# Kernel optimization log

Hardware: AMD Instinct MI355X
Metric: run time of the kernel (lower is better)

The kernel has to match this reference:

```python
import jax, jax.numpy as jnp
import numpy as np

SCOPE = 27
RICKER_WIDTH = 6.0
DAMPING = 0.12
IN_CHANNELS = 256


def _ricker(scope, std, damping):
    # mexican-hat / ricker wavelet, length `scope`, centered
    x = jnp.arange(scope, dtype=jnp.float32) - (scope // 2)
    a = 2.0 / (jnp.sqrt(3.0 * std) * jnp.pi ** 0.25)
    return damping * a * (1.0 - (x / std) ** 2) * jnp.exp(-(x ** 2) / (2.0 * std ** 2))


def _pad_roll(k, in_channels):
    # zero-pad kernel (length scope) to in_channels, roll so center sits at i=0-ish
    scope = k.shape[-1]
    pad_left = (in_channels - scope) // 2
    pad_right = in_channels - scope - pad_left
    padded = jnp.concatenate([jnp.zeros((pad_left,), k.dtype), k, jnp.zeros((pad_right,), k.dtype)])
    return jnp.roll(padded, in_channels // 2 + 1)


def _circulant(kernel, c):
    # tpl[i, j] = kernel[(j - i) mod C]  (each row is the kernel rolled by i)
    idx = (jnp.arange(c)[None, :] - jnp.arange(c)[:, None]) % c
    return kernel[idx]


def setup_inputs() -> dict:
    key = jax.random.key(0)
    k1, _ = jax.random.split(key)
    activations = jax.random.normal(k1, (32, IN_CHANNELS, 64, 64), dtype=jnp.float32)
    inhibition_filter = _ricker(SCOPE, RICKER_WIDTH, DAMPING)  # learned param, ricker init
    return {"activations": activations, "inhibition_filter": inhibition_filter}


def reference(activations, inhibition_filter):
    n, c, h, w = activations.shape
    kernel = _pad_roll(inhibition_filter, c)              # [C]
    tpl = _circulant(kernel, c)                           # [C, C]
    tpl_inv = jnp.linalg.inv(jnp.eye(c, dtype=tpl.dtype) - tpl)  # [C, C]
    # torch: (N, H*W, C) @ tpl_inv -> out[n, c_out, h, w] = sum_k act[n, k, h, w] * tpl_inv[k, c_out]
    return jnp.einsum('nkhw,kc->nchw', activations, tpl_inv)
```

## Files before the change

### kernel.cpp

```cpp
#include <hip/hip_runtime.h>
#include <hip/hip_bf16.h>

#define C 256
#define HW 4096
#define REP_ROW 528
#define LDSK 264

typedef __attribute__((ext_vector_type(8))) short short8;
typedef __attribute__((ext_vector_type(4))) float float4v;

__device__ __forceinline__ unsigned short f2bf(float x) {
    unsigned u = __builtin_bit_cast(unsigned, x);
    u = (u + 0x7fffu + ((u >> 16) & 1u)) >> 16;
    return (unsigned short)u;
}

__global__ void build_rep_kernel(const float* __restrict__ filt, unsigned short* __restrict__ rep) {
    __shared__ double twc[256], tws[256];
    __shared__ double Gre[256], Gim[256];
    __shared__ float gsh[256];
    const int t = threadIdx.x;
    const double PI = 3.14159265358979323846;
    double th = (double)t * (PI / 128.0);
    twc[t] = cos(th);
    tws[t] = sin(th);
    __syncthreads();
    double re = 1.0, im = 0.0;
    for (int i = 0; i < 27; ++i) {
        int d = (243 + i) & 255;
        int idx = (t * d) & 255;
        double fv = (double)filt[i];
        re -= fv * twc[idx];
        im += fv * tws[idx];
    }
    double den = re * re + im * im;
    Gre[t] = re / den;
    Gim[t] = -im / den;
    __syncthreads();
    double acc = 0.0;
    for (int f = 0; f < 256; ++f) {
        int idx = (f * t) & 255;
        acc += Gre[f] * twc[idx] - Gim[f] * tws[idx];
    }
    gsh[t] = (float)(acc * (1.0 / 256.0));
    __syncthreads();
    for (int e = t; e < 8 * REP_ROW; e += 256) {
        int tt = e / REP_ROW, u = e % REP_ROW;
        int src = (4096 - u - tt) & 255;
        rep[e] = f2bf(gsh[src]);
    }
}

__global__ __launch_bounds__(256, 2)
void toeplitz_gemm_kernel(const float* __restrict__ act,
                          const unsigned short* __restrict__ rep_g,
                          float* __restrict__ out) {
    __shared__ unsigned short rep[8 * REP_ROW];
    __shared__ unsigned short atile[64 * LDSK];

    const int tid = threadIdx.x;
    const int wave = tid >> 6;
    const int lane = tid & 63;
    const int m = lane & 15;
    const int quad = lane >> 4;
    const int blk = blockIdx.x;
    const int n = blk >> 6;
    const int p0 = (blk & 63) << 6;
    const float* actn = act + (size_t)n * (C * HW);
    float* outn = out + (size_t)n * (C * HW);

    {
        const uint4* rg = (const uint4*)rep_g;
        uint4* rl = (uint4*)rep;
        for (int i = tid; i < (8 * REP_ROW * 2) / 16; i += 256) rl[i] = rg[i];
    }

    {
        const int kb = (tid & 15) << 2;
        const int pb = (tid >> 4) << 2;
#pragma unroll
        for (int it = 0; it < 4; ++it) {
            const int ks = it * 64 + kb;
            const float* g0 = actn + (size_t)ks * HW + p0 + pb;
            float4v r0 = *(const float4v*)(g0);
            float4v r1 = *(const float4v*)(g0 + HW);
            float4v r2 = *(const float4v*)(g0 + 2 * HW);
            float4v r3 = *(const float4v*)(g0 + 3 * HW);
#pragma unroll
            for (int pp = 0; pp < 4; ++pp) {
                unsigned long long pk =
                      (unsigned long long)f2bf(r0[pp])
                    | ((unsigned long long)f2bf(r1[pp]) << 16)
                    | ((unsigned long long)f2bf(r2[pp]) << 32)
                    | ((unsigned long long)f2bf(r3[pp]) << 48);
                *(unsigned long long*)&atile[(pb + pp) * LDSK + ks] = pk;
            }
        }
    }
    __syncthreads();

    short8 afrag[16];
#pragma unroll
    for (int f = 0; f < 16; ++f) {
        int s = ((f - 4 * wave) & 15) << 4;
        int e = s + 256 + quad * 8 - m;
        int tt = e & 7, q = e >> 3;
        afrag[f] = *(const short8*)&rep[tt * REP_ROW + q * 8];
    }

    float4v acc[4][4];
#pragma unroll
    for (int ct = 0; ct < 4; ++ct)
#pragma unroll
        for (int pt = 0; pt < 4; ++pt)
            acc[ct][pt] = (float4v){0.f, 0.f, 0.f, 0.f};

#pragma unroll
    for (int a = 0; a < 8; ++a) {
        const int k0 = a * 32;
        short8 bfr[4];
#pragma unroll
        for (int pt = 0; pt < 4; ++pt) {
            const int prow = pt * 16 + m;
            bfr[pt] = *(const short8*)&atile[prow * LDSK + k0 + quad * 8];
        }
#pragma unroll
        for (int ct = 0; ct < 4; ++ct) {
            const int f = (2 * a - ct) & 15;
#pragma unroll
            for (int pt = 0; pt < 4; ++pt) {
                acc[ct][pt] = __builtin_amdgcn_mfma_f32_16x16x32_bf16(
                    afrag[f], bfr[pt], acc[ct][pt], 0, 0, 0);
            }
        }
    }

#pragma unroll
    for (int ct = 0; ct < 4; ++ct) {
#pragma unroll
        for (int r = 0; r < 4; ++r) {
            const int c = wave * 64 + ct * 16 + quad * 4 + r;
            float* op = outn + (size_t)c * HW + p0;
#pragma unroll
            for (int pt = 0; pt < 4; ++pt) {
                op[pt * 16 + m] = acc[ct][pt][r];
            }
        }
    }
}

extern "C" void kernel_launch(void* const* d_in, const int* in_sizes, int n_in,
                              void* d_out, int out_size, void* d_ws, size_t ws_size,
                              hipStream_t stream) {
    const float* act = (const float*)d_in[0];
    const float* filt = (const float*)d_in[1];
    float* out = (float*)d_out;
    unsigned short* rep = (unsigned short*)d_ws;

    build_rep_kernel<<<1, 256, 0, stream>>>(filt, rep);
    toeplitz_gemm_kernel<<<2048, 256, 0, stream>>>(act, rep, out);
}
```

Baseline: 263.4 us.

## Load Toeplitz A-fragments from LDS per step to cut registers and raise occupancy

Drops the 16 persistent A-fragment registers and instead reads the needed circulant fragments from a compacted LDS replica (REP_ROW 528 to 288) inside the K loop. This lowers VGPR pressure so launch bounds can go from 2 to 3 blocks per CU. Activation loads are batched eight at a time for more memory-level parallelism, and the setup kernel now uses float instead of double. The cost is extra LDS reads per MFMA step, plus slightly lower precision in the inverse-filter computation.

```diff
diff --git a/kernel.cpp b/kernel.cpp
--- a/kernel.cpp
+++ b/kernel.cpp
@@ -3,7 +3,7 @@
 
 #define C 256
 #define HW 4096
-#define REP_ROW 528
+#define REP_ROW 288
 #define LDSK 264
 
 typedef __attribute__((ext_vector_type(8))) short short8;
@@ -16,46 +16,46 @@
 }
 
 __global__ void build_rep_kernel(const float* __restrict__ filt, unsigned short* __restrict__ rep) {
-    __shared__ double twc[256], tws[256];
-    __shared__ double Gre[256], Gim[256];
+    __shared__ float twc[256], tws[256];
+    __shared__ float Gre[256], Gim[256];
     __shared__ float gsh[256];
     const int t = threadIdx.x;
     const double PI = 3.14159265358979323846;
     double th = (double)t * (PI / 128.0);
-    twc[t] = cos(th);
-    tws[t] = sin(th);
+    twc[t] = (float)cos(th);
+    tws[t] = (float)sin(th);
     __syncthreads();
-    double re = 1.0, im = 0.0;
+    float re = 1.0f, im = 0.0f;
     for (int i = 0; i < 27; ++i) {
         int d = (243 + i) & 255;
         int idx = (t * d) & 255;
-        double fv = (double)filt[i];
+        float fv = filt[i];
         re -= fv * twc[idx];
         im += fv * tws[idx];
     }
-    double den = re * re + im * im;
+    float den = re * re + im * im;
     Gre[t] = re / den;
     Gim[t] = -im / den;
     __syncthreads();
-    double acc = 0.0;
+    float acc = 0.0f;
     for (int f = 0; f < 256; ++f) {
         int idx = (f * t) & 255;
         acc += Gre[f] * twc[idx] - Gim[f] * tws[idx];
     }
-    gsh[t] = (float)(acc * (1.0 / 256.0));
+    gsh[t] = acc * (1.0f / 256.0f);
     __syncthreads();
     for (int e = t; e < 8 * REP_ROW; e += 256) {
-        int tt = e / REP_ROW, u = e % REP_ROW;
-        int src = (4096 - u - tt) & 255;
+        int row = e / REP_ROW, u = e - row * REP_ROW;
+        int src = (16 - u - row) & 255;
         rep[e] = f2bf(gsh[src]);
     }
 }
 
-__global__ __launch_bounds__(256, 2)
+__global__ __launch_bounds__(256, 3)
 void toeplitz_gemm_kernel(const float* __restrict__ act,
                           const unsigned short* __restrict__ rep_g,
                           float* __restrict__ out) {
-    __shared__ unsigned short rep[8 * REP_ROW];
+    __shared__ unsigned short rep2[8 * REP_ROW];
     __shared__ unsigned short atile[64 * LDSK];
 
     const int tid = threadIdx.x;
@@ -71,7 +71,7 @@
 
     {
         const uint4* rg = (const uint4*)rep_g;
-        uint4* rl = (uint4*)rep;
+        uint4* rl = (uint4*)rep2;
         for (int i = tid; i < (8 * REP_ROW * 2) / 16; i += 256) rl[i] = rg[i];
     }
 
@@ -79,34 +79,35 @@
         const int kb = (tid & 15) << 2;
         const int pb = (tid >> 4) << 2;
 #pragma unroll
-        for (int it = 0; it < 4; ++it) {
-            const int ks = it * 64 + kb;
-            const float* g0 = actn + (size_t)ks * HW + p0 + pb;
-            float4v r0 = *(const float4v*)(g0);
-            float4v r1 = *(const float4v*)(g0 + HW);
-            float4v r2 = *(const float4v*)(g0 + 2 * HW);
-            float4v r3 = *(const float4v*)(g0 + 3 * HW);
+        for (int half = 0; half < 2; ++half) {
+            float4v r[8];
 #pragma unroll
-            for (int pp = 0; pp < 4; ++pp) {
-                unsigned long long pk =
-                      (unsigned long long)f2bf(r0[pp])
-                    | ((unsigned long long)f2bf(r1[pp]) << 16)
-                    | ((unsigned long long)f2bf(r2[pp]) << 32)
-                    | ((unsigned long long)f2bf(r3[pp]) << 48);
-                *(unsigned long long*)&atile[(pb + pp) * LDSK + ks] = pk;
+            for (int it = 0; it < 2; ++it) {
+                const int ks = (half * 2 + it) * 64 + kb;
+                const float* g0 = actn + (size_t)ks * HW + p0 + pb;
+#pragma unroll
+                for (int j = 0; j < 4; ++j)
+                    r[it * 4 + j] = *(const float4v*)(g0 + (size_t)j * HW);
+            }
+#pragma unroll
+            for (int it = 0; it < 2; ++it) {
+                const int ks = (half * 2 + it) * 64 + kb;
+#pragma unroll
+                for (int pp = 0; pp < 4; ++pp) {
+                    unsigned long long pk =
+                          (unsigned long long)f2bf(r[it * 4 + 0][pp])
+                        | ((unsigned long long)f2bf(r[it * 4 + 1][pp]) << 16)
+                        | ((unsigned long long)f2bf(r[it * 4 + 2][pp]) << 32)
+                        | ((unsigned long long)f2bf(r[it * 4 + 3][pp]) << 48);
+                    *(unsigned long long*)&atile[(pb + pp) * LDSK + ks] = pk;
+                }
             }
         }
     }
     __syncthreads();
 
-    short8 afrag[16];
-#pragma unroll
-    for (int f = 0; f < 16; ++f) {
-        int s = ((f - 4 * wave) & 15) << 4;
-        int e = s + 256 + quad * 8 - m;
-        int tt = e & 7, q = e >> 3;
-        afrag[f] = *(const short8*)&rep[tt * REP_ROW + q * 8];
-    }
+    const int arow = (-m) & 7;
+    const int abase = arow * 287 + 16 + quad * 8 - m;
 
     float4v acc[4][4];
 #pragma unroll
@@ -124,13 +125,19 @@
             const int prow = pt * 16 + m;
             bfr[pt] = *(const short8*)&atile[prow * LDSK + k0 + quad * 8];
         }
+        short8 afr[4];
 #pragma unroll
         for (int ct = 0; ct < 4; ++ct) {
             const int f = (2 * a - ct) & 15;
+            const int sp = (f - 4 * wave) & 15;
+            afr[ct] = *(const short8*)&rep2[abase + (sp << 4)];
+        }
+#pragma unroll
+        for (int ct = 0; ct < 4; ++ct) {
 #pragma unroll
             for (int pt = 0; pt < 4; ++pt) {
                 acc[ct][pt] = __builtin_amdgcn_mfma_f32_16x16x32_bf16(
-                    afrag[f], bfr[pt], acc[ct][pt], 0, 0, 0);
+                    afr[ct], bfr[pt], acc[ct][pt], 0, 0, 0);
             }
         }
     }
```

Measured after the change: 256.2 us. 2.7% less time.
